# Optimization experiments

Hardware: AMD Instinct MI355X
Metric: run time of the kernel (lower is better)

The kernel has to match this reference:

```python
import jax, jax.numpy as jnp
import numpy as np

HIDDEN = 1024
HEADS = 16
HEAD_DIM = HIDDEN // HEADS
ROTARY_PCT = 0.25
ROTARY_DIM = int(HEAD_DIM * ROTARY_PCT)  # 16
BASE = 10000.0
SCALE = HEAD_DIM ** -0.5
EPS = 1e-8


def _rotate_half(x):
    h = x.shape[-1] // 2
    return jnp.concatenate([-x[..., h:], x[..., :h]], axis=-1)


def _apply_rope(q, k, position_ids):
    # q, k: [B, H, S, D]; NeoX-style partial rotary on first ROTARY_DIM dims
    inv_freq = 1.0 / (BASE ** (jnp.arange(0, ROTARY_DIM, 2, dtype=jnp.float32) / ROTARY_DIM))
    freqs = position_ids.astype(jnp.float32)[:, None] * inv_freq[None, :]  # [S, rd/2]
    emb = jnp.concatenate([freqs, freqs], axis=-1)  # [S, rd]
    cos = jnp.cos(emb)[None, None, :, :]
    sin = jnp.sin(emb)[None, None, :, :]

    def rot(x):
        x_rot, x_pass = x[..., :ROTARY_DIM], x[..., ROTARY_DIM:]
        x_rot = x_rot * cos + _rotate_half(x_rot) * sin
        return jnp.concatenate([x_rot, x_pass], axis=-1)

    return rot(q), rot(k)


def _ka_scan(attn_weights, value):
    # attn_weights: [B, H, S, S] causal softmax; value: [B, H, S, D]
    # A[0] = V[0]; A[i] = renorm(attn_weights[i, :i]) @ A[:i]
    S = value.shape[2]
    idx = jnp.arange(S)

    def step(a_buf, i):
        w = attn_weights[:, :, i, :]                      # [B, H, S]
        w = jnp.where(idx[None, None, :] < i, w, 0.0)     # strict past only
        w = w / (jnp.sum(w, axis=-1, keepdims=True) + EPS)
        a_i = jnp.einsum('bhs,bhsd->bhd', w, a_buf)
        a_i = jnp.where(i == 0, value[:, :, 0, :], a_i)
        a_buf = jax.lax.dynamic_update_slice(a_buf, a_i[:, :, None, :], (0, 0, i, 0))
        return a_buf, None

    a_buf, _ = jax.lax.scan(step, jnp.zeros_like(value), jnp.arange(S))
    return a_buf


def setup_inputs() -> dict:
    key = jax.random.key(0)
    k1, k2, k3 = jax.random.split(key, 3)
    B, S = 2, 2048
    hidden_states = jax.random.normal(k1, (B, S, HIDDEN), dtype=jnp.float32)
    position_ids = jnp.arange(S, dtype=jnp.int32)
    Wqkv = jax.random.normal(k2, (HIDDEN, 3 * HIDDEN), dtype=jnp.float32) / np.sqrt(HIDDEN)
    bqkv = jnp.zeros((3 * HIDDEN,), dtype=jnp.float32)
    Wd = jax.random.normal(k3, (HIDDEN, HIDDEN), dtype=jnp.float32) / np.sqrt(HIDDEN)
    bd = jnp.zeros((HIDDEN,), dtype=jnp.float32)
    return {"hidden_states": hidden_states, "position_ids": position_ids,
            "Wqkv": Wqkv, "bqkv": bqkv, "Wd": Wd, "bd": bd}


def reference(hidden_states, position_ids, Wqkv, bqkv, Wd, bd):
    B, S, _ = hidden_states.shape
    qkv = hidden_states @ Wqkv + bqkv                       # [B, S, 3*hidden]
    qkv = qkv.reshape(B, S, 3, HEADS, HEAD_DIM).transpose(2, 0, 3, 1, 4)
    query, key, value = qkv[0], qkv[1], qkv[2]              # [B, H, S, D]
    query, key = _apply_rope(query, key, position_ids)

    scores = jnp.einsum('bhqd,bhkd->bhqk', query, key) * SCALE
    causal = jnp.tril(jnp.ones((S, S), dtype=bool))
    scores = jnp.where(causal[None, None], scores, -jnp.inf)
    attn_weights = jax.nn.softmax(scores, axis=-1)          # [B, H, S, S]

    attn_output = _ka_scan(attn_weights, value)             # [B, H, S, D]
    attn_output = attn_output.transpose(0, 2, 1, 3).reshape(B, S, HIDDEN)
    return attn_output @ Wd + bd
```

## Files before the change

### kernel.cpp

```cpp
#include <hip/hip_runtime.h>

#define S_ 2048
#define EPSF 1e-8f
#define SCALEF 0.125f

typedef short bf16x8 __attribute__((ext_vector_type(8)));
typedef float f32x4 __attribute__((ext_vector_type(4)));

__device__ __forceinline__ unsigned short f2bf(float f){
  unsigned int u = __float_as_uint(f);
  u = (u + 0x7fffu + ((u >> 16) & 1u)) >> 16;
  return (unsigned short)u;
}
__device__ __forceinline__ float bf2f(unsigned short h){
  return __uint_as_float(((unsigned int)h) << 16);
}
__device__ __forceinline__ unsigned short f2bf_trunc(float f){
  return (unsigned short)(__float_as_uint(f) >> 16);
}

#define GLD16(g, l) __builtin_amdgcn_global_load_lds( \
    (const __attribute__((address_space(1))) unsigned int*)(g), \
    (__attribute__((address_space(3))) unsigned int*)(l), 16, 0, 0)

__global__ void k_prep(const float* __restrict__ hs, const float* __restrict__ Wqkv,
                       const float* __restrict__ bqkv, const float* __restrict__ Wd,
                       unsigned short* __restrict__ Ab,
                       unsigned short* __restrict__ WT,
                       float* __restrict__ U,
                       float* __restrict__ c_c){
  __shared__ float t[32][33];
  __shared__ float red[4][64];
  __shared__ float vsh[64];
  int bid = blockIdx.x;
  if (bid < 32){
    int bh = bid; int b = bh >> 4, h = bh & 15;
    int d = threadIdx.x & 63, kc = threadIdx.x >> 6;
    const float* x = hs + (size_t)b * S_ * 1024;
    int col = 2048 + h*64 + d;
    float acc = 0.f;
    #pragma unroll 16
    for (int k = kc*256; k < kc*256 + 256; ++k)
      acc = fmaf(x[k], Wqkv[(size_t)k*3072 + col], acc);
    red[kc][d] = acc;
    __syncthreads();
    if (kc == 0)
      vsh[d] = red[0][d] + red[1][d] + red[2][d] + red[3][d] + bqkv[col];
    __syncthreads();
    for (int n = threadIdx.x; n < 1024; n += 256){
      float a2 = 0.f;
      #pragma unroll 16
      for (int dd = 0; dd < 64; ++dd)
        a2 = fmaf(vsh[dd], Wd[(size_t)(h*64 + dd)*1024 + n], a2);
      U[(size_t)bh*1024 + n] = a2;
    }
  } else if (bid < 96){
    int q = bid - 32;
    float4 z = (float4){0.f,0.f,0.f,0.f};
    *(float4*)(c_c + (size_t)q*1024 + threadIdx.x*4) = z;
  } else if (bid < 4192){
    int i = ((bid - 96) * 256 + threadIdx.x) * 4;
    float4 v = *(const float4*)(hs + i);
    ushort4 o; o.x=f2bf(v.x); o.y=f2bf(v.y); o.z=f2bf(v.z); o.w=f2bf(v.w);
    *(ushort4*)(Ab + i) = o;
  } else {
    int q = bid - 4192;
    int nt = q & 63, kt = q >> 6;
    int tx = threadIdx.x & 31, ty = threadIdx.x >> 5;
    #pragma unroll
    for (int r = 0; r < 32; r += 8)
      t[ty + r][tx] = Wqkv[(size_t)(kt*32 + ty + r)*3072 + nt*32 + tx];
    __syncthreads();
    #pragma unroll
    for (int r = 0; r < 32; r += 8)
      WT[(size_t)(nt*32 + ty + r)*1024 + kt*32 + tx] = f2bf(t[tx][ty + r]);
  }
}

#define BK 32
__launch_bounds__(256)
__global__ void k_gemm_qk(const unsigned short* __restrict__ Ab,
                          const unsigned short* __restrict__ WT,
                          const float* __restrict__ bqkv,
                          const int* __restrict__ pos_ids,
                          unsigned short* __restrict__ Qb,
                          unsigned short* __restrict__ Kb){
  __shared__ unsigned short At[128*BK];
  __shared__ unsigned short Bt[128*BK];
  const int m0 = blockIdx.y * 128, n0 = blockIdx.x * 128;
  const int w = threadIdx.x >> 6, l = threadIdx.x & 63;
  const int wr = w >> 1, wc = w & 1;
  const int lq = l & 15, lh = l >> 4;
  f32x4 acc[4][4];
  #pragma unroll
  for (int i = 0; i < 4; ++i)
    #pragma unroll
    for (int j = 0; j < 4; ++j) acc[i][j] = (f32x4){0.f,0.f,0.f,0.f};

  const int srow = l >> 2;
  const int scol = (l & 3) * 8;

  for (int kt = 0; kt < 1024; kt += BK){
    GLD16(Ab + (size_t)(m0 + w*32 +      srow)*1024 + kt + scol, &At[(w*32)*BK]);
    GLD16(Ab + (size_t)(m0 + w*32 + 16 + srow)*1024 + kt + scol, &At[(w*32+16)*BK]);
    GLD16(WT + (size_t)(n0 + w*32 +      srow)*1024 + kt + scol, &Bt[(w*32)*BK]);
    GLD16(WT + (size_t)(n0 + w*32 + 16 + srow)*1024 + kt + scol, &Bt[(w*32+16)*BK]);
    __syncthreads();
    bf16x8 af[4], bf[4];
    #pragma unroll
    for (int i = 0; i < 4; ++i)
      af[i] = *(const bf16x8*)&At[(wr*64 + i*16 + lq)*BK + lh*8];
    #pragma unroll
    for (int j = 0; j < 4; ++j)
      bf[j] = *(const bf16x8*)&Bt[(wc*64 + j*16 + lq)*BK + lh*8];
    #pragma unroll
    for (int i = 0; i < 4; ++i)
      #pragma unroll
      for (int j = 0; j < 4; ++j)
        acc[i][j] = __builtin_amdgcn_mfma_f32_16x16x32_bf16(af[i], bf[j], acc[i][j], 0, 0, 0);
    __syncthreads();
  }
  #pragma unroll
  for (int i = 0; i < 4; ++i){
    #pragma unroll
    for (int j = 0; j < 4; ++j){
      #pragma unroll
      for (int r = 0; r < 4; ++r){
        int m = m0 + wr*64 + i*16 + (l>>4)*4 + r;
        int n = n0 + wc*64 + j*16 + (l&15);
        float v = acc[i][j][r] + bqkv[n];
        if (j == 0){
          float partner = __shfl_xor(v, 8);
          int s = m & 2047;
          float pos = (float)pos_ids[s];
          float fr = exp2f(-1.6609640474436813f * (float)(l & 7));
          float th = pos * fr;
          float sn = __sinf(th), cn = __cosf(th);
          v = ((l & 8) == 0) ? (v*cn - partner*sn) : (v*cn + partner*sn);
        }
        int b = m >> 11, s2 = m & 2047;
        int tsel = n >> 10; int nq = n & 1023;
        int h = nq >> 6, d = nq & 63;
        unsigned short* dst = tsel ? Kb : Qb;
        dst[((size_t)(b*16 + h)*S_ + s2)*64 + d] = f2bf(v);
      }
    }
  }
}

#define KST2 66
#define EST 68
__launch_bounds__(256, 4)
__global__ void k_scores(const unsigned short* __restrict__ Qb,
                         const unsigned short* __restrict__ Kb,
                         unsigned short* __restrict__ Eg,
                         float* __restrict__ rinvg){
  __shared__ unsigned short Ks[2][64*KST2];
  __shared__ unsigned short Es[4][16*EST];
  __shared__ float dsh[4][16];
  const int q = blockIdx.x >> 5, bh = blockIdx.x & 31;
  const int qm = q & 7, qk = q >> 3;
  const int bi = (qk == 0) ? qm : (qk == 1) ? (15 - qm)
               : (qk == 2) ? (16 + qm) : (31 - qm);
  const unsigned short* Qh = Qb + (size_t)bh * S_ * 64;
  const unsigned short* Kh = Kb + (size_t)bh * S_ * 64;
  const int tid = threadIdx.x, w = tid >> 6, l = tid & 63;
  const int lq = l & 15, lh = l >> 4;
  const unsigned short* qp = Qh + (size_t)(bi*64 + w*16 + lq)*64 + lh*8;
  bf16x8 qf0 = *(const bf16x8*)(qp);
  bf16x8 qf1 = *(const bf16x8*)(qp + 32);
  float dacc[4] = {0.f,0.f,0.f,0.f};
  unsigned short* Etile0 = Eg + ((size_t)bh*528 + (size_t)(bi*(bi+1)/2))*4096;
  const int srow = tid >> 2, sc = (tid & 3)*16;

  {
    const unsigned short* src = Kh + (size_t)srow*64 + sc;
    *(int4*)&Ks[0][srow*KST2 + sc]     = *(const int4*)(src);
    *(int4*)&Ks[0][srow*KST2 + sc + 8] = *(const int4*)(src + 8);
  }
  __syncthreads();

  for (int bj = 0; bj <= bi; ++bj){
    const int cur = bj & 1;
    int4 nk0, nk1;
    if (bj < bi){
      const unsigned short* src = Kh + (size_t)((bj+1)*64 + srow)*64 + sc;
      nk0 = *(const int4*)(src);
      nk1 = *(const int4*)(src + 8);
    }
    unsigned short* Et = Etile0 + (size_t)bj*4096 + w*1024;
    const bool diag = (bj == bi);
    #pragma unroll
    for (int ct = 0; ct < 4; ++ct){
      bf16x8 b0 = *(const bf16x8*)&Ks[cur][(ct*16 + lq)*KST2 + lh*8];
      bf16x8 b1 = *(const bf16x8*)&Ks[cur][(ct*16 + lq)*KST2 + 32 + lh*8];
      f32x4 a = (f32x4){0.f,0.f,0.f,0.f};
      a = __builtin_amdgcn_mfma_f32_16x16x32_bf16(qf0, b0, a, 0, 0, 0);
      a = __builtin_amdgcn_mfma_f32_16x16x32_bf16(qf1, b1, a, 0, 0, 0);
      #pragma unroll
      for (int r = 0; r < 4; ++r){
        float e = __expf(a[r] * SCALEF);
        unsigned short eb = f2bf_trunc(e);
        int rrow = lh*4 + r, col = ct*16 + lq;
        Es[w][rrow*EST + col] = eb;
        float ev = bf2f(eb);
        int grow = w*16 + rrow;
        if (!diag || col < grow) dacc[r] += ev;
        if (diag && col == grow) dsh[w][rrow] = ev;
      }
    }
    #pragma unroll
    for (int it = 0; it < 2; ++it){
      int row = it*8 + (l >> 3), eo = (l & 7)*8;
      *(int4*)(Et + row*64 + eo) = *(const int4*)&Es[w][row*EST + eo];
    }
    if (bj < bi){
      *(int4*)&Ks[cur^1][srow*KST2 + sc]     = nk0;
      *(int4*)&Ks[cur^1][srow*KST2 + sc + 8] = nk1;
    }
    __syncthreads();
  }
  #pragma unroll
  for (int r = 0; r < 4; ++r){
    float d = dacc[r];
    #pragma unroll
    for (int mm = 1; mm < 16; mm <<= 1) d += __shfl_xor(d, mm);
    float dE = dsh[w][lh*4 + r];
    float den = fmaf(EPSF, d + dE, d);
    float rv = 1.0f / den;
    if (lq == 0)
      rinvg[(size_t)bh*S_ + bi*64 + w*16 + lh*4 + r] = rv;
  }
}

__global__ __launch_bounds__(64)
void k_dinv(const unsigned short* __restrict__ Eg,
            const float* __restrict__ rinvg,
            unsigned short* __restrict__ Dg){
  __shared__ float As[64*65];
  const int bh = blockIdx.x >> 5, bi = blockIdx.x & 31;
  const unsigned short* Et =
      Eg + ((size_t)bh*528 + (size_t)(bi*(bi+1)/2) + bi)*4096;
  const int c = threadIdx.x;
  for (int r = 0; r < 64; ++r){
    float rv = rinvg[(size_t)bh*S_ + bi*64 + r];
    float e = bf2f(Et[(r>>4)*1024 + (r&15)*64 + c]);
    As[r*65 + c] = (c < r) ? e * rv : 0.f;
  }
  __syncthreads();
  float X[64];
  #pragma unroll
  for (int r = 0; r < 64; ++r){
    float acc = (r == c) ? 1.f : 0.f;
    #pragma unroll
    for (int k = 0; k < r; ++k)
      acc = fmaf(As[r*65 + k], X[k], acc);
    X[r] = acc;
  }
  unsigned short* dt = Dg + (size_t)blockIdx.x * 4096;
  #pragma unroll
  for (int r = 0; r < 64; ++r)
    dt[(r>>4)*1024 + (r&15)*64 + c] = f2bf(X[r]);
}

__global__ __launch_bounds__(512)
__attribute__((amdgpu_waves_per_eu(2, 2)))
void k_recur3(const unsigned short* __restrict__ Eg,
              const unsigned short* __restrict__ Dg,
              const float* __restrict__ rinvg,
              float* __restrict__ c_c,
              float* __restrict__ c_g){
  __shared__ float Pa[256];
  __shared__ float rso[256];
  __shared__ float csl[2][64];
  __shared__ float bb[64];
  const int bh = blockIdx.x & 31, s = blockIdx.x >> 5;
  const unsigned short* Eh = Eg + (size_t)bh * 528 * 4096;
  const int tid = threadIdx.x, w = tid >> 6, l = tid & 63;
  const int lq = l & 15, lh = l >> 4;

  if (tid < 256){
    Pa[tid] = 0.f;
    rso[tid] = rinvg[(size_t)bh*S_ + (s + 8*(tid >> 6))*64 + l];
  }
  __syncthreads();

  bf16x8 dv0[4], dv1[4];
  if (w == 0){
    const unsigned short* dt = Dg + (size_t)(bh*32 + s)*4096;
    #pragma unroll
    for (int q = 0; q < 4; ++q){
      dv0[q] = *(const bf16x8*)(dt + q*1024 + lq*64 + lh*8);
      dv1[q] = *(const bf16x8*)(dt + q*1024 + lq*64 + 32 + lh*8);
    }
  }

  bf16x8 dA0[3], dA1[3], dB0[3], dB1[3];
  bf16x8 ug0, ug1;
  const int lastc = s + 24;

  auto load_def = [&](int BJ, bf16x8 (&D0)[3], bf16x8 (&D1)[3]){
    int o0 = (BJ >= s) ? (((BJ - s) >> 3) + 1) : 0;
    int ex = (((BJ + 1) & 7) == s) ? 1 : 0;
    int nd = (4 - o0 - ex) * 4;
    if (w >= 1){
      #pragma unroll
      for (int k = 0; k < 3; ++k){
        int t = (w - 1) + k*7;
        if (t < nd){
          int ob = o0 + ex + (t >> 2);
          int bi = s + 8*ob;
          const unsigned short* tp =
              Eh + ((size_t)(bi*(bi+1)/2) + BJ)*4096 + (size_t)(t & 3)*1024;
          D0[k] = *(const bf16x8*)(tp + lq*64 + lh*8);
          D1[k] = *(const bf16x8*)(tp + lq*64 + 32 + lh*8);
        }
      }
      if (ex && w <= 4){
        int bi = BJ + 1;
        const unsigned short* tp =
            Eh + ((size_t)(bi*(bi+1)/2) + BJ)*4096 + (size_t)(w-1)*1024;
        ug0 = *(const bf16x8*)(tp + lq*64 + lh*8);
        ug1 = *(const bf16x8*)(tp + lq*64 + 32 + lh*8);
      }
    }
  };

  auto fold_def = [&](int BJP, bf16x8 (&D0)[3], bf16x8 (&D1)[3], int buf){
    int o0 = (BJP >= s) ? (((BJP - s) >> 3) + 1) : 0;
    int ex = (((BJP + 1) & 7) == s) ? 1 : 0;
    int nd = (4 - o0 - ex) * 4;
    if (w >= 1 && nd > 0){
      bf16x8 dc0 = (bf16x8){0,0,0,0,0,0,0,0};
      bf16x8 dc1 = (bf16x8){0,0,0,0,0,0,0,0};
      if (lq == 0){
        #pragma unroll
        for (int e = 0; e < 8; ++e){
          dc0[e] = (short)f2bf(csl[buf][lh*8 + e]);
          dc1[e] = (short)f2bf(csl[buf][32 + lh*8 + e]);
        }
      }
      #pragma unroll
      for (int k = 0; k < 3; ++k){
        int t = (w - 1) + k*7;
        if (t < nd){
          f32x4 o = (f32x4){0.f,0.f,0.f,0.f};
          o = __builtin_amdgcn_mfma_f32_16x16x32_bf16(D0[k], dc0, o, 0, 0, 0);
          o = __builtin_amdgcn_mfma_f32_16x16x32_bf16(D1[k], dc1, o, 0, 0, 0);
          if (lq == 0){
            int ob = o0 + ex + (t >> 2);
            float* base = Pa + ob*64 + (t & 3)*16 + lh*4;
            float4 v = *(float4*)base;
            v.x += o[0]; v.y += o[1]; v.z += o[2]; v.w += o[3];
            *(float4*)base = v;
          }
        }
      }
    }
  };

  auto iter = [&](int BJ, bf16x8 (&DL0)[3], bf16x8 (&DL1)[3],
                          bf16x8 (&DF0)[3], bf16x8 (&DF1)[3]){
    const int cur = BJ & 1;
    load_def(BJ, DL0, DL1);
    const int ex = (((BJ + 1) & 7) == s) ? 1 : 0;
    if (w == 0){
      if ((BJ & 7) == s){
        const int o = (BJ - s) >> 3;
        float bval = rso[o*64 + l] * Pa[o*64 + l];
        if (BJ == 0 && l == 0) bval = 1.0f;
        bb[l] = bval;
        bf16x8 uc0 = (bf16x8){0,0,0,0,0,0,0,0};
        bf16x8 uc1 = (bf16x8){0,0,0,0,0,0,0,0};
        if (lq == 0){
          #pragma unroll
          for (int e = 0; e < 8; ++e){
            uc0[e] = (short)f2bf(bb[lh*8 + e]);
            uc1[e] = (short)f2bf(bb[32 + lh*8 + e]);
          }
        }
        #pragma unroll
        for (int q = 0; q < 4; ++q){
          f32x4 o4 = (f32x4){0.f,0.f,0.f,0.f};
          o4 = __builtin_amdgcn_mfma_f32_16x16x32_bf16(dv0[q], uc0, o4, 0, 0, 0);
          o4 = __builtin_amdgcn_mfma_f32_16x16x32_bf16(dv1[q], uc1, o4, 0, 0, 0);
          if (lq == 0){
            #pragma unroll
            for (int r = 0; r < 4; ++r)
              csl[cur][q*16 + lh*4 + r] = o4[r];
          }
        }
        float cval = csl[cur][l];
        __hip_atomic_store((unsigned*)(c_c + (size_t)bh*S_ + BJ*64 + l),
                           __float_as_uint(cval),
                           __ATOMIC_RELAXED, __HIP_MEMORY_SCOPE_AGENT);
        c_g[((size_t)(bh >> 4)*S_ + (BJ*64 + l))*16 + (bh & 15)] = cval;
        int bn = BJ + 8;
        if (bn <= lastc){
          const unsigned short* dt = Dg + (size_t)(bh*32 + bn)*4096;
          #pragma unroll
          for (int q = 0; q < 4; ++q){
            dv0[q] = *(const bf16x8*)(dt + q*1024 + lq*64 + lh*8);
            dv1[q] = *(const bf16x8*)(dt + q*1024 + lq*64 + 32 + lh*8);
          }
        }
      } else {
        const unsigned* pp = (const unsigned*)(c_c + (size_t)bh*S_ + BJ*64 + l);
        unsigned v = __hip_atomic_load(pp, __ATOMIC_RELAXED,
                                       __HIP_MEMORY_SCOPE_AGENT);
        while (!__all(v != 0u)){
          __builtin_amdgcn_s_sleep(2);
          v = __hip_atomic_load(pp, __ATOMIC_RELAXED,
                                __HIP_MEMORY_SCOPE_AGENT);
        }
        csl[cur][l] = __uint_as_float(v);
      }
    } else if (BJ >= 1){
      fold_def(BJ - 1, DF0, DF1, cur ^ 1);
    }
    __syncthreads();
    if (ex && w >= 1 && w <= 4){
      bf16x8 uc0 = (bf16x8){0,0,0,0,0,0,0,0};
      bf16x8 uc1 = (bf16x8){0,0,0,0,0,0,0,0};
      if (lq == 0){
        #pragma unroll
        for (int e = 0; e < 8; ++e){
          uc0[e] = (short)f2bf(csl[cur][lh*8 + e]);
          uc1[e] = (short)f2bf(csl[cur][32 + lh*8 + e]);
        }
      }
      f32x4 o = (f32x4){0.f,0.f,0.f,0.f};
      o = __builtin_amdgcn_mfma_f32_16x16x32_bf16(ug0, uc0, o, 0, 0, 0);
      o = __builtin_amdgcn_mfma_f32_16x16x32_bf16(ug1, uc1, o, 0, 0, 0);
      if (lq == 0){
        int ou = (BJ + 1 - s) >> 3;
        float* base = Pa + ou*64 + (w-1)*16 + lh*4;
        float4 v = *(float4*)base;
        v.x += o[0]; v.y += o[1]; v.z += o[2]; v.w += o[3];
        *(float4*)base = v;
      }
    }
    __syncthreads();
  };

  for (int bj = 0; bj <= lastc; bj += 2){
    iter(bj,     dA0, dA1, dB0, dB1);
    if (bj + 1 <= lastc)
      iter(bj+1, dB0, dB1, dA0, dA1);
  }
}

__global__ void k_out(const float* __restrict__ c_g, const float* __restrict__ U,
                      const float* __restrict__ bd, float* __restrict__ out){
  int bs = blockIdx.x; int b = bs >> 11;
  __shared__ float ch[16];
  if (threadIdx.x < 16) ch[threadIdx.x] = c_g[(size_t)bs*16 + threadIdx.x];
  __syncthreads();
  int n = threadIdx.x * 4;
  float4 acc = *(const float4*)(bd + n);
  #pragma unroll
  for (int h = 0; h < 16; ++h){
    float cc = ch[h];
    float4 u = *(const float4*)(U + ((size_t)(b*16 + h))*1024 + n);
    acc.x = fmaf(cc, u.x, acc.x); acc.y = fmaf(cc, u.y, acc.y);
    acc.z = fmaf(cc, u.z, acc.z); acc.w = fmaf(cc, u.w, acc.w);
  }
  *(float4*)(out + (size_t)bs*1024 + n) = acc;
}

extern "C" void kernel_launch(void* const* d_in, const int* in_sizes, int n_in,
                              void* d_out, int out_size, void* d_ws, size_t ws_size,
                              hipStream_t stream) {
  const float* hs   = (const float*)d_in[0];
  const int*   pos  = (const int*)d_in[1];
  const float* Wqkv = (const float*)d_in[2];
  const float* bqkv = (const float*)d_in[3];
  const float* Wd   = (const float*)d_in[4];
  const float* bd   = (const float*)d_in[5];
  float* out = (float*)d_out;

  char* ws = (char*)d_ws;
  unsigned short* Ab = (unsigned short*)(ws);
  unsigned short* Dg = (unsigned short*)(ws);
  unsigned short* WT = (unsigned short*)(ws + (8u<<20));
  unsigned short* Qb = (unsigned short*)(ws + (12u<<20));
  unsigned short* Kb = (unsigned short*)(ws + (20u<<20));
  float* c_g  = (float*)(ws + (28u<<20) + 0x10000);
  float* U    = (float*)(ws + (28u<<20) + 0x50000);
  float* rinvg= (float*)(ws + (28u<<20) + 0x80000);
  float* c_c  = (float*)(ws + (28u<<20) + 0xC0000);
  unsigned short* Eg = (unsigned short*)(ws + (29u<<20));

  k_prep   <<<6240, 256, 0, stream>>>(hs, Wqkv, bqkv, Wd, Ab, WT, U, c_c);
  k_gemm_qk<<<dim3(16, 32), 256, 0, stream>>>(Ab, WT, bqkv, pos, Qb, Kb);
  k_scores <<<1024, 256, 0, stream>>>(Qb, Kb, Eg, rinvg);
  k_dinv   <<<1024, 64, 0, stream>>>(Eg, rinvg, Dg);
  k_recur3 <<<256, 512, 0, stream>>>(Eg, Dg, rinvg, c_c, c_g);
  k_out    <<<4096, 256, 0, stream>>>(c_g, U, bd, out);
}
```

Before: 169.0 us.

## Move urgent-block fold to owner warp and drop second per-iteration barrier

The urgent next-block tile (the ex case) is no longer loaded and folded by warps 1-4 after a mid-iteration barrier. Warp 0 now prefetches the whole 64x64 tile into registers and folds it itself at the start of its owning iteration, using the previous step's c values. This removes one __syncthreads per iteration from the serial scan's critical path. Warps 1+ now issue their deferred loads after the fold, the spin-wait sleep is shortened, and warp 0 carries extra registers and MFMA work on the critical path.

```diff
diff --git a/kernel.cpp b/kernel.cpp
--- a/kernel.cpp
+++ b/kernel.cpp
@@ -286,6 +286,7 @@
   __syncthreads();
 
   bf16x8 dv0[4], dv1[4];
+  bf16x8 ug0[4], ug1[4];
   if (w == 0){
     const unsigned short* dt = Dg + (size_t)(bh*32 + s)*4096;
     #pragma unroll
@@ -296,32 +297,22 @@
   }
 
   bf16x8 dA0[3], dA1[3], dB0[3], dB1[3];
-  bf16x8 ug0, ug1;
   const int lastc = s + 24;
 
   auto load_def = [&](int BJ, bf16x8 (&D0)[3], bf16x8 (&D1)[3]){
     int o0 = (BJ >= s) ? (((BJ - s) >> 3) + 1) : 0;
     int ex = (((BJ + 1) & 7) == s) ? 1 : 0;
     int nd = (4 - o0 - ex) * 4;
-    if (w >= 1){
-      #pragma unroll
-      for (int k = 0; k < 3; ++k){
-        int t = (w - 1) + k*7;
-        if (t < nd){
-          int ob = o0 + ex + (t >> 2);
-          int bi = s + 8*ob;
-          const unsigned short* tp =
-              Eh + ((size_t)(bi*(bi+1)/2) + BJ)*4096 + (size_t)(t & 3)*1024;
-          D0[k] = *(const bf16x8*)(tp + lq*64 + lh*8);
-          D1[k] = *(const bf16x8*)(tp + lq*64 + 32 + lh*8);
-        }
-      }
-      if (ex && w <= 4){
-        int bi = BJ + 1;
+    #pragma unroll
+    for (int k = 0; k < 3; ++k){
+      int t = (w - 1) + k*7;
+      if (t < nd){
+        int ob = o0 + ex + (t >> 2);
+        int bi = s + 8*ob;
         const unsigned short* tp =
-            Eh + ((size_t)(bi*(bi+1)/2) + BJ)*4096 + (size_t)(w-1)*1024;
-        ug0 = *(const bf16x8*)(tp + lq*64 + lh*8);
-        ug1 = *(const bf16x8*)(tp + lq*64 + 32 + lh*8);
+            Eh + ((size_t)(bi*(bi+1)/2) + BJ)*4096 + (size_t)(t & 3)*1024;
+        D0[k] = *(const bf16x8*)(tp + lq*64 + lh*8);
+        D1[k] = *(const bf16x8*)(tp + lq*64 + 32 + lh*8);
       }
     }
   };
@@ -330,7 +321,7 @@
     int o0 = (BJP >= s) ? (((BJP - s) >> 3) + 1) : 0;
     int ex = (((BJP + 1) & 7) == s) ? 1 : 0;
     int nd = (4 - o0 - ex) * 4;
-    if (w >= 1 && nd > 0){
+    if (nd > 0){
       bf16x8 dc0 = (bf16x8){0,0,0,0,0,0,0,0};
       bf16x8 dc1 = (bf16x8){0,0,0,0,0,0,0,0};
       if (lq == 0){
@@ -362,10 +353,43 @@
   auto iter = [&](int BJ, bf16x8 (&DL0)[3], bf16x8 (&DL1)[3],
                           bf16x8 (&DF0)[3], bf16x8 (&DF1)[3]){
     const int cur = BJ & 1;
-    load_def(BJ, DL0, DL1);
     const int ex = (((BJ + 1) & 7) == s) ? 1 : 0;
+    const bool own = ((BJ & 7) == s);
     if (w == 0){
-      if ((BJ & 7) == s){
+      if (own && BJ >= 1){
+        bf16x8 uc0 = (bf16x8){0,0,0,0,0,0,0,0};
+        bf16x8 uc1 = (bf16x8){0,0,0,0,0,0,0,0};
+        if (lq == 0){
+          #pragma unroll
+          for (int e = 0; e < 8; ++e){
+            uc0[e] = (short)f2bf(csl[cur^1][lh*8 + e]);
+            uc1[e] = (short)f2bf(csl[cur^1][32 + lh*8 + e]);
+          }
+        }
+        const int o = (BJ - s) >> 3;
+        #pragma unroll
+        for (int q = 0; q < 4; ++q){
+          f32x4 o4 = (f32x4){0.f,0.f,0.f,0.f};
+          o4 = __builtin_amdgcn_mfma_f32_16x16x32_bf16(ug0[q], uc0, o4, 0, 0, 0);
+          o4 = __builtin_amdgcn_mfma_f32_16x16x32_bf16(ug1[q], uc1, o4, 0, 0, 0);
+          if (lq == 0){
+            float* base = Pa + o*64 + q*16 + lh*4;
+            float4 v = *(float4*)base;
+            v.x += o4[0]; v.y += o4[1]; v.z += o4[2]; v.w += o4[3];
+            *(float4*)base = v;
+          }
+        }
+      }
+      if (ex){
+        int bi = BJ + 1;
+        const unsigned short* tp = Eh + ((size_t)(bi*(bi+1)/2) + BJ)*4096;
+        #pragma unroll
+        for (int q = 0; q < 4; ++q){
+          ug0[q] = *(const bf16x8*)(tp + q*1024 + lq*64 + lh*8);
+          ug1[q] = *(const bf16x8*)(tp + q*1024 + lq*64 + 32 + lh*8);
+        }
+      }
+      if (own){
         const int o = (BJ - s) >> 3;
         float bval = rso[o*64 + l] * Pa[o*64 + l];
         if (BJ == 0 && l == 0) bval = 1.0f;
@@ -409,36 +433,15 @@
         unsigned v = __hip_atomic_load(pp, __ATOMIC_RELAXED,
                                        __HIP_MEMORY_SCOPE_AGENT);
         while (!__all(v != 0u)){
-          __builtin_amdgcn_s_sleep(2);
+          __builtin_amdgcn_s_sleep(1);
           v = __hip_atomic_load(pp, __ATOMIC_RELAXED,
                                 __HIP_MEMORY_SCOPE_AGENT);
         }
         csl[cur][l] = __uint_as_float(v);
       }
-    } else if (BJ >= 1){
-      fold_def(BJ - 1, DF0, DF1, cur ^ 1);
-    }
-    __syncthreads();
-    if (ex && w >= 1 && w <= 4){
-      bf16x8 uc0 = (bf16x8){0,0,0,0,0,0,0,0};
-      bf16x8 uc1 = (bf16x8){0,0,0,0,0,0,0,0};
-      if (lq == 0){
-        #pragma unroll
-        for (int e = 0; e < 8; ++e){
-          uc0[e] = (short)f2bf(csl[cur][lh*8 + e]);
-          uc1[e] = (short)f2bf(csl[cur][32 + lh*8 + e]);
-        }
-      }
-      f32x4 o = (f32x4){0.f,0.f,0.f,0.f};
-      o = __builtin_amdgcn_mfma_f32_16x16x32_bf16(ug0, uc0, o, 0, 0, 0);
-      o = __builtin_amdgcn_mfma_f32_16x16x32_bf16(ug1, uc1, o, 0, 0, 0);
-      if (lq == 0){
-        int ou = (BJ + 1 - s) >> 3;
-        float* base = Pa + ou*64 + (w-1)*16 + lh*4;
-        float4 v = *(float4*)base;
-        v.x += o[0]; v.y += o[1]; v.z += o[2]; v.w += o[3];
-        *(float4*)base = v;
-      }
+    } else {
+      if (BJ >= 1) fold_def(BJ - 1, DF0, DF1, cur ^ 1);
+      load_def(BJ, DL0, DL1);
     }
     __syncthreads();
   };
```

Result: no change. 172.2 us, median of 3 (+1.9%).
